# Kernel optimization log

Hardware: AMD Instinct MI355X
Metric: run time of the kernel (lower is better)

The kernel has to match this reference:

```python
import jax, jax.numpy as jnp
import numpy as np
from jax import lax

V, T, B, E, H, L, K = 32000, 256, 32, 512, 256, 2, 17  # vocab, seq, batch, emb, hidden/dir, layers, tags


def _lstm_dir(x, mask, Wih, Whh, bih, bhh, reverse):
    """One-direction LSTM with packed-sequence semantics.
    x: [B,T,D], mask: [B,T] bool. Padded steps do not update (h,c); padded outputs are 0."""
    Bs, Ts, _ = x.shape
    Hs = Whh.shape[1]
    xg = jnp.einsum('btd,gd->btg', x, Wih) + bih  # precompute input contributions [B,T,4H]

    def step(carry, inp):
        h, c = carry
        xg_t, m_t = inp  # [B,4H], [B]
        g = xg_t + h @ Whh.T + bhh
        i, f, gg, o = jnp.split(g, 4, axis=-1)  # torch gate order: i, f, g, o
        i = jax.nn.sigmoid(i); f = jax.nn.sigmoid(f)
        gg = jnp.tanh(gg); o = jax.nn.sigmoid(o)
        c_new = f * c + i * gg
        h_new = o * jnp.tanh(c_new)
        m = m_t[:, None]
        h2 = jnp.where(m, h_new, h)
        c2 = jnp.where(m, c_new, c)
        out = jnp.where(m, h_new, jnp.zeros_like(h_new))
        return (h2, c2), out

    z = jnp.zeros((Bs, Hs), dtype=x.dtype)
    xs = (jnp.swapaxes(xg, 0, 1), mask.T)
    _, ys = lax.scan(step, (z, z), xs, reverse=reverse)
    return jnp.swapaxes(ys, 0, 1)  # [B,T,H]


def _bilstm(x, mask, Wih, Whh, bih, bhh):
    for l in range(Wih.shape[0]):
        f = _lstm_dir(x, mask, Wih[l, 0], Whh[l, 0], bih[l, 0], bhh[l, 0], reverse=False)
        b = _lstm_dir(x, mask, Wih[l, 1], Whh[l, 1], bih[l, 1], bhh[l, 1], reverse=True)
        x = jnp.concatenate([f, b], axis=-1)
    return x


def _crf_nll(logits, labels, mask, input_lens, trans, start, end):
    maskf = mask.astype(logits.dtype)
    # --- numerator: score of gold path (AllenNLP _joint_likelihood) ---
    emit = jnp.take_along_axis(logits, labels[..., None], axis=2)[..., 0]  # [B,T]
    emit_sum = (emit * maskf).sum(1)
    tr = trans[labels[:, :-1], labels[:, 1:]]  # [B,T-1]
    tr_sum = (tr * maskf[:, 1:]).sum(1)
    last_tags = jnp.take_along_axis(labels, (input_lens - 1)[:, None], axis=1)[:, 0]
    numerator = start[labels[:, 0]] + emit_sum + tr_sum + end[last_tags]
    # --- denominator: forward algorithm over time ---
    alpha0 = start[None, :] + logits[:, 0]  # [B,K]

    def step(alpha, inp):
        logit_t, m_t = inp  # [B,K], [B]
        inner = alpha[:, :, None] + trans[None] + logit_t[:, None, :]  # [B,K,K]
        new = jax.nn.logsumexp(inner, axis=1)
        alpha = jnp.where(m_t[:, None], new, alpha)
        return alpha, None

    xs = (jnp.swapaxes(logits[:, 1:], 0, 1), mask[:, 1:].T)
    alpha, _ = lax.scan(step, alpha0, xs)
    partition = jax.nn.logsumexp(alpha + end[None, :], axis=1)
    return -(numerator - partition).sum()


def setup_inputs() -> dict:
    key = jax.random.key(0)
    ks = jax.random.split(key, 10)
    lens = jax.random.randint(ks[0], (B,), 1, T + 1)
    src = jax.random.randint(ks[1], (B, T), 1, V)
    src = jnp.where(jnp.arange(T)[None, :] < lens[:, None], src, 0)  # pad_idx=0
    labels = jax.random.randint(ks[2], (B, T), 0, K)
    emb = (jax.random.normal(ks[3], (V, E)) * 0.05).at[0].set(0.0)  # padding_idx=0 row zeroed
    Wih = jax.random.normal(ks[4], (L, 2, 4 * H, E)) * 0.05
    Whh = jax.random.normal(ks[5], (L, 2, 4 * H, H)) * 0.05
    bih = jnp.zeros((L, 2, 4 * H))
    bhh = jnp.zeros((L, 2, 4 * H))
    Wlin = jax.random.normal(ks[6], (K, 2 * H)) * 0.05
    blin = jnp.zeros((K,))
    trans = jax.random.normal(ks[7], (K, K)) * 0.05
    start = jax.random.normal(ks[8], (K,)) * 0.05
    end = jax.random.normal(ks[9], (K,)) * 0.05
    return dict(src=src, input_lens=lens, labels=labels, decode=0, emb=emb,
                Wih=Wih, Whh=Whh, bih=bih, bhh=bhh, Wlin=Wlin, blin=blin,
                trans=trans, start=start, end=end)


def reference(src, input_lens, labels, decode, emb, Wih, Whh, bih, bhh, Wlin, blin, trans, start, end):
    mask = src != 0  # create_mask with pad_idx=0
    x = emb[src]  # embedding lookup (dropout p=0 -> identity)
    feats = _bilstm(x, mask, Wih, Whh, bih, bhh)
    logits = feats @ Wlin.T + blin  # [B,T,K]
    # decode=False path: loss = -crf log-likelihood (summed over batch)
    return _crf_nll(logits, labels, mask, input_lens, trans, start, end)
```

## Files before the change

### kernel.cpp

```cpp
#include <hip/hip_runtime.h>

#define TT 256
#define BB 32
#define EE 512
#define HH 256
#define GG 1024
#define NK 17

typedef __attribute__((ext_vector_type(8))) short bf16x8;
typedef __attribute__((ext_vector_type(4))) float f32x4;

#if __has_builtin(__builtin_amdgcn_sdot8)
#define HAS_DOT8 1
#else
#define HAS_DOT8 0
#endif

__device__ __forceinline__ int dot4i8(int a, int b, int c) {
#if __has_builtin(__builtin_amdgcn_sdot4)
  return __builtin_amdgcn_sdot4(a, b, c, false);
#else
  int r = c;
#pragma unroll
  for (int e = 0; e < 4; ++e) {
    int av = (a << (24 - 8 * e)) >> 24;
    int bv = (b << (24 - 8 * e)) >> 24;
    r += av * bv;
  }
  return r;
#endif
}

__device__ __forceinline__ int dot8i4(int a, int b, int c) {
#if HAS_DOT8
  return __builtin_amdgcn_sdot8(a, b, c, false);
#else
  int alo = (a << 4) & (int)0xF0F0F0F0, ahi = a & (int)0xF0F0F0F0;
  int blo = (b << 4) & (int)0xF0F0F0F0, bhi = b & (int)0xF0F0F0F0;
  c = dot4i8(alo, blo, c);
  return dot4i8(ahi, bhi, c);
#endif
}

__device__ __forceinline__ short f2bf(float f) {
  unsigned int u = __float_as_uint(f);
  unsigned int rounding = 0x7FFFu + ((u >> 16) & 1u);
  return (short)((u + rounding) >> 16);
}
__device__ __forceinline__ float bfu2f_lo(unsigned int u) {
  return __uint_as_float(u << 16);
}
__device__ __forceinline__ float bfu2f_hi(unsigned int u) {
  return __uint_as_float(u & 0xFFFF0000u);
}
__device__ __forceinline__ float bfs2f(unsigned short us) {
  return __uint_as_float(((unsigned int)us) << 16);
}

__global__ void k_embed(const int* __restrict__ src,
                        const float* __restrict__ emb,
                        short* __restrict__ xb) {
  int row = blockIdx.x;
  int v = src[row];
  int t = threadIdx.x;
  const float4* e = reinterpret_cast<const float4*>(emb + (size_t)v * EE) + 2 * t;
  float4 a = e[0], b = e[1];
  bf16x8 r;
  r[0] = f2bf(a.x); r[1] = f2bf(a.y); r[2] = f2bf(a.z); r[3] = f2bf(a.w);
  r[4] = f2bf(b.x); r[5] = f2bf(b.y); r[6] = f2bf(b.z); r[7] = f2bf(b.w);
  *reinterpret_cast<bf16x8*>(xb + (size_t)row * EE + 8 * t) = r;
}

__global__ __launch_bounds__(256) void k_cvt(const float* __restrict__ in,
                                             short* __restrict__ out) {
  int i = (blockIdx.x * 256 + threadIdx.x) * 8;
  float4 a = *reinterpret_cast<const float4*>(in + i);
  float4 b = *reinterpret_cast<const float4*>(in + i + 4);
  bf16x8 r;
  r[0] = f2bf(a.x); r[1] = f2bf(a.y); r[2] = f2bf(a.z); r[3] = f2bf(a.w);
  r[4] = f2bf(b.x); r[5] = f2bf(b.y); r[6] = f2bf(b.z); r[7] = f2bf(b.w);
  *reinterpret_cast<bf16x8*>(out + i) = r;
}

__global__ __launch_bounds__(256) void k_quant4(const float* __restrict__ whh,
                                                const float* __restrict__ bih,
                                                const float* __restrict__ bhh,
                                                int* __restrict__ wq4,
                                                float* __restrict__ scl,
                                                float* __restrict__ biasb) {
  int wid = (blockIdx.x * 256 + threadIdx.x) >> 6;
  int lane = threadIdx.x & 63;
  int ld = wid >> 10, g = wid & 1023;
  float4 v = *reinterpret_cast<const float4*>(whh + (size_t)wid * HH + lane * 4);
  float m = fmaxf(fmaxf(fabsf(v.x), fabsf(v.y)), fmaxf(fabsf(v.z), fabsf(v.w)));
#pragma unroll
  for (int off = 32; off > 0; off >>= 1) m = fmaxf(m, __shfl_xor(m, off));
  m = fmaxf(m, 1e-20f);
  float inv = 7.f / m;
  unsigned q0 = (unsigned)((int)rintf(v.x * inv) & 0xF);
  unsigned q1 = (unsigned)((int)rintf(v.y * inv) & 0xF);
  unsigned q2 = (unsigned)((int)rintf(v.z * inv) & 0xF);
  unsigned q3 = (unsigned)((int)rintf(v.w * inv) & 0xF);
  unsigned bits = q0 | (q1 << 4) | (q2 << 8) | (q3 << 12);
  unsigned hi = __shfl_down(bits, 1);
  if (!(lane & 1)) {
    int kk = lane >> 1;
    wq4[(((size_t)ld * 8 + (kk >> 2)) * 1024 + g) * 4 + (kk & 3)] =
        (int)(bits | (hi << 16));
  }
  if (lane == 0) scl[wid] = m / 49.f;
  if (lane == 1) biasb[wid] = bih[wid] + bhh[wid];
}

__global__ __launch_bounds__(256) void k_gemm_mfma(
    const short* __restrict__ Xb,
    const short* __restrict__ Wb,
    const float* __restrict__ bias,
    unsigned short* __restrict__ out) {
  __shared__ short As[128][72];
  __shared__ short Bs[128][72];
  const int tid = threadIdx.x;
  const int wave = tid >> 6, lane = tid & 63;
  const int wr = wave >> 1, wc = wave & 1;
  const int m0 = blockIdx.y * 128, n0 = blockIdx.x * 128;
  f32x4 acc[4][4] = {};
  for (int k0 = 0; k0 < EE; k0 += 64) {
#pragma unroll
    for (int u = 0; u < 4; ++u) {
      int cid = u * 256 + tid;
      int row = cid >> 3, kc = cid & 7;
      *reinterpret_cast<int4*>(&As[row][kc * 8]) =
          *reinterpret_cast<const int4*>(Xb + (size_t)(m0 + row) * EE + k0 + kc * 8);
      *reinterpret_cast<int4*>(&Bs[row][kc * 8]) =
          *reinterpret_cast<const int4*>(Wb + (size_t)(n0 + row) * EE + k0 + kc * 8);
    }
    __syncthreads();
#pragma unroll
    for (int ko = 0; ko < 2; ++ko) {
      bf16x8 af[4], bff[4];
#pragma unroll
      for (int mi = 0; mi < 4; ++mi)
        af[mi] = *reinterpret_cast<const bf16x8*>(
            &As[wr * 64 + mi * 16 + (lane & 15)][ko * 32 + (lane >> 4) * 8]);
#pragma unroll
      for (int ni = 0; ni < 4; ++ni)
        bff[ni] = *reinterpret_cast<const bf16x8*>(
            &Bs[wc * 64 + ni * 16 + (lane & 15)][ko * 32 + (lane >> 4) * 8]);
#pragma unroll
      for (int mi = 0; mi < 4; ++mi)
#pragma unroll
        for (int ni = 0; ni < 4; ++ni)
          acc[mi][ni] = __builtin_amdgcn_mfma_f32_16x16x32_bf16(af[mi], bff[ni], acc[mi][ni], 0, 0, 0);
    }
    __syncthreads();
  }
  const int r0 = (lane >> 4) * 4, cc = lane & 15;
#pragma unroll
  for (int mi = 0; mi < 4; ++mi)
#pragma unroll
    for (int ni = 0; ni < 4; ++ni) {
      int gcol = n0 + wc * 64 + ni * 16 + cc;
      int dir = gcol >> 10, gg = gcol & 1023;
      float bv = bias[gcol];
      unsigned short* ob = out + (size_t)dir * (BB * TT * GG) + gg;
#pragma unroll
      for (int j = 0; j < 4; ++j) {
        int m = m0 + wr * 64 + mi * 16 + r0 + j;
        ob[(size_t)m * GG] = (unsigned short)f2bf(acc[mi][ni][j] + bv);
      }
    }
}

__global__ __launch_bounds__(1024) void k_rec(
    const unsigned short* __restrict__ xg,
    const uint4* __restrict__ wq4,
    const float* __restrict__ scl,
    const int* __restrict__ lens,
    short* __restrict__ outx)
{
  __shared__ __align__(16) int hq[32];
  const int bid = blockIdx.x;
  const int b = bid & 31;
  const int dir = bid >> 5;
  const int g = threadIdx.x;
  const uint4* wp = wq4 + (size_t)dir * (8 * 1024) + g;
  if (g < 32) hq[g] = 0;
#if HAS_DOT8
  const float f = scl[dir * 1024 + g];
#else
  const float f = scl[dir * 1024 + g] * (1.f / 256.f);
#endif
  __shared__ float pre[GG];
  const int len = lens[b];
  const unsigned short* xgb = xg + ((size_t)dir * (BB * TT) + (size_t)b * TT) * GG + g;
  float c = 0.f;
  __syncthreads();
  for (int s = 0; s < TT; ++s) {
    const int t = dir ? (TT - 1 - s) : s;
    float xv = bfs2f(xgb[(size_t)t * GG]);
    const uint4* h4 = reinterpret_cast<const uint4*>(hq);
    uint4 hv0 = h4[0], hv1 = h4[1], hv2 = h4[2], hv3 = h4[3];
    uint4 hv4 = h4[4], hv5 = h4[5], hv6 = h4[6], hv7 = h4[7];
    int acc = 0;
#define DOTQ(Q, HV)                                \
    { uint4 wv = wp[(Q) * 1024];                   \
      acc = dot8i4((int)wv.x, (int)HV.x, acc);     \
      acc = dot8i4((int)wv.y, (int)HV.y, acc);     \
      acc = dot8i4((int)wv.z, (int)HV.z, acc);     \
      acc = dot8i4((int)wv.w, (int)HV.w, acc); }
    DOTQ(0, hv0) DOTQ(1, hv1) DOTQ(2, hv2) DOTQ(3, hv3)
    DOTQ(4, hv4) DOTQ(5, hv5) DOTQ(6, hv6) DOTQ(7, hv7)
#undef DOTQ
    pre[g] = xv + (float)acc * f;
    __syncthreads();
    if (g < HH) {
      float gi = pre[g], gf = pre[HH + g], g2 = pre[2 * HH + g], go = pre[3 * HH + g];
      float iv = 1.f / (1.f + __expf(-gi));
      float fv = 1.f / (1.f + __expf(-gf));
      float e2 = __expf(fminf(2.f * g2, 80.f));
      float gv = (e2 - 1.f) / (e2 + 1.f);
      float ov = 1.f / (1.f + __expf(-go));
      float cn = fv * c + iv * gv;
      float e2c = __expf(fminf(2.f * cn, 80.f));
      float th = (e2c - 1.f) / (e2c + 1.f);
      float hn = ov * th;
      const bool m = (t < len);
      outx[((size_t)(b * TT) + t) * (2 * HH) + dir * HH + g] = f2bf(m ? hn : 0.f);
      if (m) {
        c = cn;
        int nib = ((int)rintf(hn * 7.f)) & 0xF;
        int pn = __shfl_xor(nib, 1);
        if (!(g & 1))
          reinterpret_cast<char*>(hq)[g >> 1] = (char)(nib | (pn << 4));
      }
    }
    __syncthreads();
  }
}

__global__ __launch_bounds__(256) void k_logits(
    const short* __restrict__ feats,
    const float* __restrict__ wlin,
    const float* __restrict__ blin,
    float* __restrict__ logits) {
  int o = blockIdx.x * 256 + threadIdx.x;
  int m = o / NK, jj = o - m * NK;
  const uint4* fr = reinterpret_cast<const uint4*>(feats + (size_t)m * EE);
  const float4* wr = reinterpret_cast<const float4*>(wlin + (size_t)jj * EE);
  float s = blin[jj];
  for (int q = 0; q < EE / 8; ++q) {
    uint4 fv = fr[q];
    float4 w0 = wr[2 * q], w1 = wr[2 * q + 1];
    s = fmaf(bfu2f_lo(fv.x), w0.x, s);
    s = fmaf(bfu2f_hi(fv.x), w0.y, s);
    s = fmaf(bfu2f_lo(fv.y), w0.z, s);
    s = fmaf(bfu2f_hi(fv.y), w0.w, s);
    s = fmaf(bfu2f_lo(fv.z), w1.x, s);
    s = fmaf(bfu2f_hi(fv.z), w1.y, s);
    s = fmaf(bfu2f_lo(fv.w), w1.z, s);
    s = fmaf(bfu2f_hi(fv.w), w1.w, s);
  }
  logits[o] = s;
}

__global__ __launch_bounds__(64) void k_crf(
    const float* __restrict__ logits,
    const int* __restrict__ labels,
    const int* __restrict__ lens,
    const float* __restrict__ trans,
    const float* __restrict__ startv,
    const float* __restrict__ endv,
    float* __restrict__ res) {
  const int b = blockIdx.x;
  const int tid = threadIdx.x;
  __shared__ float trs[NK * NK];
  __shared__ float alpha[NK];
  for (int i = tid; i < NK * NK; i += 64) trs[i] = trans[i];
  const int len = lens[b];
  const int* lab = labels + b * TT;
  const float* lg = logits + (size_t)b * TT * NK;
  float part = 0.f;
  for (int t = tid; t < TT; t += 64)
    if (t < len) part += lg[t * NK + lab[t]];
  for (int t = tid; t < TT - 1; t += 64)
    if (t + 1 < len) part += trs[lab[t] * NK + lab[t + 1]];
#pragma unroll
  for (int off = 32; off > 0; off >>= 1) part += __shfl_down(part, off);
  if (tid < NK) alpha[tid] = startv[tid] + lg[tid];
  const int tmax = (len < TT) ? len : TT;
  for (int t = 1; t < tmax; ++t) {
    float nv = 0.f;
    if (tid < NK) {
      float mxv = -1e30f;
#pragma unroll
      for (int i = 0; i < NK; ++i) mxv = fmaxf(mxv, alpha[i] + trs[i * NK + tid]);
      float sum = 0.f;
#pragma unroll
      for (int i = 0; i < NK; ++i) sum += __expf(alpha[i] + trs[i * NK + tid] - mxv);
      nv = mxv + __logf(sum) + lg[t * NK + tid];
    }
    if (tid < NK) alpha[tid] = nv;
  }
  if (tid == 0) {
    float mxv = -1e30f;
    float av[NK];
    for (int i = 0; i < NK; ++i) { av[i] = alpha[i] + endv[i]; mxv = fmaxf(mxv, av[i]); }
    float sum = 0.f;
    for (int i = 0; i < NK; ++i) sum += __expf(av[i] - mxv);
    float partition = mxv + __logf(sum);
    float numer = startv[lab[0]] + part + endv[lab[len - 1]];
    res[b] = numer - partition;
  }
}

__global__ void k_final(const float* __restrict__ res, float* __restrict__ out) {
  int tid = threadIdx.x;
  float v = (tid < BB) ? res[tid] : 0.f;
#pragma unroll
  for (int off = 32; off > 0; off >>= 1) v += __shfl_down(v, off);
  if (tid == 0) out[0] = -v;
}

extern "C" void kernel_launch(void* const* d_in, const int* in_sizes, int n_in,
                              void* d_out, int out_size, void* d_ws, size_t ws_size,
                              hipStream_t stream) {
  const int* src = (const int*)d_in[0];
  const int* lens = (const int*)d_in[1];
  const int* labels = (const int*)d_in[2];
  const float* emb = (const float*)d_in[4];
  const float* Wih = (const float*)d_in[5];
  const float* Whh = (const float*)d_in[6];
  const float* bih = (const float*)d_in[7];
  const float* bhh = (const float*)d_in[8];
  const float* Wlin = (const float*)d_in[9];
  const float* blin = (const float*)d_in[10];
  const float* trans = (const float*)d_in[11];
  const float* startv = (const float*)d_in[12];
  const float* endv = (const float*)d_in[13];

  char* w = (char*)d_ws;
  short* xb0 = (short*)w;   w += (size_t)BB * TT * EE * 2;
  short* xb1 = (short*)w;   w += (size_t)BB * TT * EE * 2;
  short* xb2 = (short*)w;   w += (size_t)BB * TT * EE * 2;
  unsigned short* xg = (unsigned short*)w; w += (size_t)2 * BB * TT * GG * 2;
  int* wq4 = (int*)w;       w += (size_t)4 * 32 * 1024 * 4;
  float* scl = (float*)w;   w += (size_t)4 * 1024 * 4;
  float* biasb = (float*)w; w += (size_t)2 * 2 * GG * 4;
  float* logits = (float*)w; w += (size_t)BB * TT * NK * 4;
  float* res = (float*)w;   w += 256;
  short* wbb = (short*)w;   w += (size_t)4 * GG * EE * 2;

  k_embed<<<BB * TT, 64, 0, stream>>>(src, emb, xb0);
  k_quant4<<<1024, 256, 0, stream>>>(Whh, bih, bhh, wq4, scl, biasb);
  k_cvt<<<(4 * GG * EE) / (256 * 8), 256, 0, stream>>>(Wih, wbb);

  const short* xin[2] = {xb0, xb1};
  short* xout[2] = {xb1, xb2};
  for (int l = 0; l < 2; ++l) {
    k_gemm_mfma<<<dim3(2 * GG / 128, (BB * TT) / 128), 256, 0, stream>>>(
        xin[l], wbb + (size_t)l * 2 * GG * EE, biasb + l * 2 * GG, xg);
    k_rec<<<64, 1024, 0, stream>>>(
        xg, reinterpret_cast<const uint4*>(wq4) + (size_t)l * 2 * 8 * 1024,
        scl + (size_t)l * 2 * 1024, lens, xout[l]);
  }

  k_logits<<<(BB * TT * NK) / 256, 256, 0, stream>>>(xb2, Wlin, blin, logits);
  k_crf<<<BB, 64, 0, stream>>>(logits, labels, lens, trans, startv, endv, res);
  k_final<<<1, 64, 0, stream>>>(res, (float*)d_out);
}
```

Measured before the change: 597.1 us.

## Keep int4 recurrent weights in registers and compute all four gates per hidden unit

```diff
diff --git a/kernel.cpp b/kernel.cpp
--- a/kernel.cpp
+++ b/kernel.cpp
@@ -91,6 +91,7 @@
   int wid = (blockIdx.x * 256 + threadIdx.x) >> 6;
   int lane = threadIdx.x & 63;
   int ld = wid >> 10, g = wid & 1023;
+  int gate = g >> 8, j = g & 255;
   float4 v = *reinterpret_cast<const float4*>(whh + (size_t)wid * HH + lane * 4);
   float m = fmaxf(fmaxf(fabsf(v.x), fabsf(v.y)), fmaxf(fabsf(v.z), fabsf(v.w)));
 #pragma unroll
@@ -105,7 +106,10 @@
   unsigned hi = __shfl_down(bits, 1);
   if (!(lane & 1)) {
     int kk = lane >> 1;
-    wq4[(((size_t)ld * 8 + (kk >> 2)) * 1024 + g) * 4 + (kk & 3)] =
+    int kq = kk >> 3, ld8 = kk & 7;
+    int tid_dest = j * 4 + kq;
+    int cch = gate * 2 + (ld8 >> 2), dw = ld8 & 3;
+    wq4[(size_t)ld * 32768 + ((size_t)(cch * 1024 + tid_dest) << 2) + dw] =
         (int)(bits | (hi << 16));
   }
   if (lane == 0) scl[wid] = m / 49.f;
@@ -178,62 +182,103 @@
     const int* __restrict__ lens,
     short* __restrict__ outx)
 {
-  __shared__ __align__(16) int hq[32];
+  __shared__ __align__(16) int hq2[2][32];
   const int bid = blockIdx.x;
   const int b = bid & 31;
   const int dir = bid >> 5;
-  const int g = threadIdx.x;
-  const uint4* wp = wq4 + (size_t)dir * (8 * 1024) + g;
-  if (g < 32) hq[g] = 0;
+  const int tid = threadIdx.x;
+  const int j = tid >> 2;
+  const uint4* wp = wq4 + (size_t)dir * 8192 + tid;
+  uint4 w0 = wp[0];
+  uint4 w1 = wp[1024];
+  uint4 w2 = wp[2048];
+  uint4 w3 = wp[3072];
+  uint4 w4 = wp[4096];
+  uint4 w5 = wp[5120];
+  uint4 w6 = wp[6144];
+  uint4 w7 = wp[7168];
+  if (tid < 64) ((int*)hq2)[tid] = 0;
 #if HAS_DOT8
-  const float f = scl[dir * 1024 + g];
+  const float fsc = 1.f;
 #else
-  const float f = scl[dir * 1024 + g] * (1.f / 256.f);
+  const float fsc = 1.f / 256.f;
 #endif
-  __shared__ float pre[GG];
+  const float s0 = scl[dir * 1024 + j] * fsc;
+  const float s1 = scl[dir * 1024 + 256 + j] * fsc;
+  const float s2 = scl[dir * 1024 + 512 + j] * fsc;
+  const float s3 = scl[dir * 1024 + 768 + j] * fsc;
   const int len = lens[b];
-  const unsigned short* xgb = xg + ((size_t)dir * (BB * TT) + (size_t)b * TT) * GG + g;
-  float c = 0.f;
+  const unsigned short* xgb = xg + ((size_t)dir * (BB * TT) + (size_t)b * TT) * GG;
+  float c = 0.f, hcur = 0.f;
   __syncthreads();
   for (int s = 0; s < TT; ++s) {
     const int t = dir ? (TT - 1 - s) : s;
-    float xv = bfs2f(xgb[(size_t)t * GG]);
-    const uint4* h4 = reinterpret_cast<const uint4*>(hq);
-    uint4 hv0 = h4[0], hv1 = h4[1], hv2 = h4[2], hv3 = h4[3];
-    uint4 hv4 = h4[4], hv5 = h4[5], hv6 = h4[6], hv7 = h4[7];
-    int acc = 0;
-#define DOTQ(Q, HV)                                \
-    { uint4 wv = wp[(Q) * 1024];                   \
-      acc = dot8i4((int)wv.x, (int)HV.x, acc);     \
-      acc = dot8i4((int)wv.y, (int)HV.y, acc);     \
-      acc = dot8i4((int)wv.z, (int)HV.z, acc);     \
-      acc = dot8i4((int)wv.w, (int)HV.w, acc); }
-    DOTQ(0, hv0) DOTQ(1, hv1) DOTQ(2, hv2) DOTQ(3, hv3)
-    DOTQ(4, hv4) DOTQ(5, hv5) DOTQ(6, hv6) DOTQ(7, hv7)
-#undef DOTQ
-    pre[g] = xv + (float)acc * f;
-    __syncthreads();
-    if (g < HH) {
-      float gi = pre[g], gf = pre[HH + g], g2 = pre[2 * HH + g], go = pre[3 * HH + g];
-      float iv = 1.f / (1.f + __expf(-gi));
-      float fv = 1.f / (1.f + __expf(-gf));
-      float e2 = __expf(fminf(2.f * g2, 80.f));
-      float gv = (e2 - 1.f) / (e2 + 1.f);
-      float ov = 1.f / (1.f + __expf(-go));
-      float cn = fv * c + iv * gv;
-      float e2c = __expf(fminf(2.f * cn, 80.f));
-      float th = (e2c - 1.f) / (e2c + 1.f);
-      float hn = ov * th;
-      const bool m = (t < len);
-      outx[((size_t)(b * TT) + t) * (2 * HH) + dir * HH + g] = f2bf(m ? hn : 0.f);
-      if (m) {
-        c = cn;
-        int nib = ((int)rintf(hn * 7.f)) & 0xF;
-        int pn = __shfl_xor(nib, 1);
-        if (!(g & 1))
-          reinterpret_cast<char*>(hq)[g >> 1] = (char)(nib | (pn << 4));
-      }
-    }
+    const unsigned short* xrow = xgb + (size_t)t * GG;
+    float xv0 = bfs2f(xrow[j]);
+    float xv1 = bfs2f(xrow[256 + j]);
+    float xv2 = bfs2f(xrow[512 + j]);
+    float xv3 = bfs2f(xrow[768 + j]);
+    const int p = s & 1;
+    const uint4* hv4 = reinterpret_cast<const uint4*>(hq2[p]);
+    uint4 h0 = hv4[(tid & 3) * 2], h1 = hv4[(tid & 3) * 2 + 1];
+    int a0 = 0, a1 = 0, a2 = 0, a3 = 0;
+    a0 = dot8i4((int)w0.x, (int)h0.x, a0);
+    a0 = dot8i4((int)w0.y, (int)h0.y, a0);
+    a0 = dot8i4((int)w0.z, (int)h0.z, a0);
+    a0 = dot8i4((int)w0.w, (int)h0.w, a0);
+    a0 = dot8i4((int)w1.x, (int)h1.x, a0);
+    a0 = dot8i4((int)w1.y, (int)h1.y, a0);
+    a0 = dot8i4((int)w1.z, (int)h1.z, a0);
+    a0 = dot8i4((int)w1.w, (int)h1.w, a0);
+    a1 = dot8i4((int)w2.x, (int)h0.x, a1);
+    a1 = dot8i4((int)w2.y, (int)h0.y, a1);
+    a1 = dot8i4((int)w2.z, (int)h0.z, a1);
+    a1 = dot8i4((int)w2.w, (int)h0.w, a1);
+    a1 = dot8i4((int)w3.x, (int)h1.x, a1);
+    a1 = dot8i4((int)w3.y, (int)h1.y, a1);
+    a1 = dot8i4((int)w3.z, (int)h1.z, a1);
+    a1 = dot8i4((int)w3.w, (int)h1.w, a1);
+    a2 = dot8i4((int)w4.x, (int)h0.x, a2);
+    a2 = dot8i4((int)w4.y, (int)h0.y, a2);
+    a2 = dot8i4((int)w4.z, (int)h0.z, a2);
+    a2 = dot8i4((int)w4.w, (int)h0.w, a2);
+    a2 = dot8i4((int)w5.x, (int)h1.x, a2);
+    a2 = dot8i4((int)w5.y, (int)h1.y, a2);
+    a2 = dot8i4((int)w5.z, (int)h1.z, a2);
+    a2 = dot8i4((int)w5.w, (int)h1.w, a2);
+    a3 = dot8i4((int)w6.x, (int)h0.x, a3);
+    a3 = dot8i4((int)w6.y, (int)h0.y, a3);
+    a3 = dot8i4((int)w6.z, (int)h0.z, a3);
+    a3 = dot8i4((int)w6.w, (int)h0.w, a3);
+    a3 = dot8i4((int)w7.x, (int)h1.x, a3);
+    a3 = dot8i4((int)w7.y, (int)h1.y, a3);
+    a3 = dot8i4((int)w7.z, (int)h1.z, a3);
+    a3 = dot8i4((int)w7.w, (int)h1.w, a3);
+    a0 += __shfl_xor(a0, 1); a0 += __shfl_xor(a0, 2);
+    a1 += __shfl_xor(a1, 1); a1 += __shfl_xor(a1, 2);
+    a2 += __shfl_xor(a2, 1); a2 += __shfl_xor(a2, 2);
+    a3 += __shfl_xor(a3, 1); a3 += __shfl_xor(a3, 2);
+    float gi = xv0 + (float)a0 * s0;
+    float gf = xv1 + (float)a1 * s1;
+    float gg = xv2 + (float)a2 * s2;
+    float go = xv3 + (float)a3 * s3;
+    float iv = 1.f / (1.f + __expf(-gi));
+    float fv = 1.f / (1.f + __expf(-gf));
+    float e2 = __expf(fminf(2.f * gg, 80.f));
+    float gv = (e2 - 1.f) / (e2 + 1.f);
+    float ov = 1.f / (1.f + __expf(-go));
+    float cn = fv * c + iv * gv;
+    float e2c = __expf(fminf(2.f * cn, 80.f));
+    float th = (e2c - 1.f) / (e2c + 1.f);
+    float hn = ov * th;
+    const bool m = (t < len);
+    if (m) { c = cn; hcur = hn; }
+    if ((tid & 3) == 0)
+      outx[((size_t)(b * TT) + t) * (2 * HH) + dir * HH + j] = f2bf(m ? hn : 0.f);
+    int nib = ((int)rintf(hcur * 7.f)) & 0xF;
+    int pn = __shfl_xor(nib, 4);
+    if ((tid & 7) == 0)
+      reinterpret_cast<char*>(hq2[p ^ 1])[tid >> 3] = (char)(nib | (pn << 4));
     __syncthreads();
   }
 }
@@ -343,7 +388,7 @@
   short* xb1 = (short*)w;   w += (size_t)BB * TT * EE * 2;
   short* xb2 = (short*)w;   w += (size_t)BB * TT * EE * 2;
   unsigned short* xg = (unsigned short*)w; w += (size_t)2 * BB * TT * GG * 2;
-  int* wq4 = (int*)w;       w += (size_t)4 * 32 * 1024 * 4;
+  int* wq4 = (int*)w;       w += (size_t)4 * 32768 * 4;
   float* scl = (float*)w;   w += (size_t)4 * 1024 * 4;
   float* biasb = (float*)w; w += (size_t)2 * 2 * GG * 4;
   float* logits = (float*)w; w += (size_t)BB * TT * NK * 4;
@@ -360,7 +405,7 @@
     k_gemm_mfma<<<dim3(2 * GG / 128, (BB * TT) / 128), 256, 0, stream>>>(
         xin[l], wbb + (size_t)l * 2 * GG * EE, biasb + l * 2 * GG, xg);
     k_rec<<<64, 1024, 0, stream>>>(
-        xg, reinterpret_cast<const uint4*>(wq4) + (size_t)l * 2 * 8 * 1024,
+        xg, reinterpret_cast<const uint4*>(wq4) + (size_t)l * 2 * 8192,
         scl + (size_t)l * 2 * 1024, lens, xout[l]);
   }
 
```

New measurement: 860.2 us. +44.1%, slower.

## Halve recurrent block size with two gate rows per thread; merge embed and weight-convert kernels

Applied to the files above, without the earlier changes.

```diff
diff --git a/kernel.cpp b/kernel.cpp
--- a/kernel.cpp
+++ b/kernel.cpp
@@ -57,29 +57,30 @@
   return __uint_as_float(((unsigned int)us) << 16);
 }
 
-__global__ void k_embed(const int* __restrict__ src,
-                        const float* __restrict__ emb,
-                        short* __restrict__ xb) {
-  int row = blockIdx.x;
-  int v = src[row];
+__global__ void k_prep_x(const int* __restrict__ src,
+                         const float* __restrict__ emb,
+                         const float* __restrict__ Wih,
+                         short* __restrict__ xb,
+                         short* __restrict__ wbb) {
+  int blk = blockIdx.x;
   int t = threadIdx.x;
-  const float4* e = reinterpret_cast<const float4*>(emb + (size_t)v * EE) + 2 * t;
-  float4 a = e[0], b = e[1];
-  bf16x8 r;
-  r[0] = f2bf(a.x); r[1] = f2bf(a.y); r[2] = f2bf(a.z); r[3] = f2bf(a.w);
-  r[4] = f2bf(b.x); r[5] = f2bf(b.y); r[6] = f2bf(b.z); r[7] = f2bf(b.w);
-  *reinterpret_cast<bf16x8*>(xb + (size_t)row * EE + 8 * t) = r;
-}
-
-__global__ __launch_bounds__(256) void k_cvt(const float* __restrict__ in,
-                                             short* __restrict__ out) {
-  int i = (blockIdx.x * 256 + threadIdx.x) * 8;
-  float4 a = *reinterpret_cast<const float4*>(in + i);
-  float4 b = *reinterpret_cast<const float4*>(in + i + 4);
-  bf16x8 r;
-  r[0] = f2bf(a.x); r[1] = f2bf(a.y); r[2] = f2bf(a.z); r[3] = f2bf(a.w);
-  r[4] = f2bf(b.x); r[5] = f2bf(b.y); r[6] = f2bf(b.z); r[7] = f2bf(b.w);
-  *reinterpret_cast<bf16x8*>(out + i) = r;
+  if (blk < BB * TT) {
+    int v = src[blk];
+    const float4* e = reinterpret_cast<const float4*>(emb + (size_t)v * EE) + 2 * t;
+    float4 a = e[0], b = e[1];
+    bf16x8 r;
+    r[0] = f2bf(a.x); r[1] = f2bf(a.y); r[2] = f2bf(a.z); r[3] = f2bf(a.w);
+    r[4] = f2bf(b.x); r[5] = f2bf(b.y); r[6] = f2bf(b.z); r[7] = f2bf(b.w);
+    *reinterpret_cast<bf16x8*>(xb + (size_t)blk * EE + 8 * t) = r;
+  } else {
+    int i = ((blk - BB * TT) * 64 + t) * 8;
+    float4 a = *reinterpret_cast<const float4*>(Wih + i);
+    float4 b = *reinterpret_cast<const float4*>(Wih + i + 4);
+    bf16x8 r;
+    r[0] = f2bf(a.x); r[1] = f2bf(a.y); r[2] = f2bf(a.z); r[3] = f2bf(a.w);
+    r[4] = f2bf(b.x); r[5] = f2bf(b.y); r[6] = f2bf(b.z); r[7] = f2bf(b.w);
+    *reinterpret_cast<bf16x8*>(wbb + i) = r;
+  }
 }
 
 __global__ __launch_bounds__(256) void k_quant4(const float* __restrict__ whh,
@@ -171,50 +172,62 @@
     }
 }
 
-__global__ __launch_bounds__(1024) void k_rec(
+__global__ __launch_bounds__(512, 2) void k_rec(
     const unsigned short* __restrict__ xg,
     const uint4* __restrict__ wq4,
     const float* __restrict__ scl,
     const int* __restrict__ lens,
     short* __restrict__ outx)
 {
+  __shared__ float pre[GG];
   __shared__ __align__(16) int hq[32];
   const int bid = blockIdx.x;
   const int b = bid & 31;
   const int dir = bid >> 5;
-  const int g = threadIdx.x;
-  const uint4* wp = wq4 + (size_t)dir * (8 * 1024) + g;
-  if (g < 32) hq[g] = 0;
+  const int L = threadIdx.x;
+  const int g0 = L, g1 = L + 512;
+  const uint4* wp0 = wq4 + (size_t)dir * (8 * 1024) + g0;
+  const uint4* wp1 = wq4 + (size_t)dir * (8 * 1024) + g1;
+  if (L < 32) hq[L] = 0;
 #if HAS_DOT8
-  const float f = scl[dir * 1024 + g];
+  const float f0 = scl[dir * 1024 + g0];
+  const float f1 = scl[dir * 1024 + g1];
 #else
-  const float f = scl[dir * 1024 + g] * (1.f / 256.f);
+  const float f0 = scl[dir * 1024 + g0] * (1.f / 256.f);
+  const float f1 = scl[dir * 1024 + g1] * (1.f / 256.f);
 #endif
-  __shared__ float pre[GG];
   const int len = lens[b];
-  const unsigned short* xgb = xg + ((size_t)dir * (BB * TT) + (size_t)b * TT) * GG + g;
+  const unsigned short* xgb = xg + ((size_t)dir * (BB * TT) + (size_t)b * TT) * GG;
   float c = 0.f;
   __syncthreads();
   for (int s = 0; s < TT; ++s) {
     const int t = dir ? (TT - 1 - s) : s;
-    float xv = bfs2f(xgb[(size_t)t * GG]);
+    float xv0 = bfs2f(xgb[(size_t)t * GG + g0]);
+    float xv1 = bfs2f(xgb[(size_t)t * GG + g1]);
     const uint4* h4 = reinterpret_cast<const uint4*>(hq);
     uint4 hv0 = h4[0], hv1 = h4[1], hv2 = h4[2], hv3 = h4[3];
     uint4 hv4 = h4[4], hv5 = h4[5], hv6 = h4[6], hv7 = h4[7];
-    int acc = 0;
-#define DOTQ(Q, HV)                                \
-    { uint4 wv = wp[(Q) * 1024];                   \
-      acc = dot8i4((int)wv.x, (int)HV.x, acc);     \
-      acc = dot8i4((int)wv.y, (int)HV.y, acc);     \
-      acc = dot8i4((int)wv.z, (int)HV.z, acc);     \
-      acc = dot8i4((int)wv.w, (int)HV.w, acc); }
-    DOTQ(0, hv0) DOTQ(1, hv1) DOTQ(2, hv2) DOTQ(3, hv3)
-    DOTQ(4, hv4) DOTQ(5, hv5) DOTQ(6, hv6) DOTQ(7, hv7)
+    int a0 = 0, a1 = 0;
+#define DOTQ(WP, ACC, Q, HV)                               \
+    { uint4 wv = WP[(Q) * 1024];                           \
+      ACC = dot8i4((int)wv.x, (int)HV.x, ACC);             \
+      ACC = dot8i4((int)wv.y, (int)HV.y, ACC);             \
+      ACC = dot8i4((int)wv.z, (int)HV.z, ACC);             \
+      ACC = dot8i4((int)wv.w, (int)HV.w, ACC); }
+    DOTQ(wp0, a0, 0, hv0) DOTQ(wp0, a0, 1, hv1)
+    DOTQ(wp0, a0, 2, hv2) DOTQ(wp0, a0, 3, hv3)
+    DOTQ(wp0, a0, 4, hv4) DOTQ(wp0, a0, 5, hv5)
+    DOTQ(wp0, a0, 6, hv6) DOTQ(wp0, a0, 7, hv7)
+    DOTQ(wp1, a1, 0, hv0) DOTQ(wp1, a1, 1, hv1)
+    DOTQ(wp1, a1, 2, hv2) DOTQ(wp1, a1, 3, hv3)
+    DOTQ(wp1, a1, 4, hv4) DOTQ(wp1, a1, 5, hv5)
+    DOTQ(wp1, a1, 6, hv6) DOTQ(wp1, a1, 7, hv7)
 #undef DOTQ
-    pre[g] = xv + (float)acc * f;
+    pre[g0] = xv0 + (float)a0 * f0;
+    pre[g1] = xv1 + (float)a1 * f1;
     __syncthreads();
-    if (g < HH) {
-      float gi = pre[g], gf = pre[HH + g], g2 = pre[2 * HH + g], go = pre[3 * HH + g];
+    if (L < HH) {
+      float gi = pre[L], gf = pre[HH + L], g2 = pre[2 * HH + L], go = pre[3 * HH + L];
       float iv = 1.f / (1.f + __expf(-gi));
       float fv = 1.f / (1.f + __expf(-gf));
       float e2 = __expf(fminf(2.f * g2, 80.f));
@@ -225,13 +238,13 @@
       float th = (e2c - 1.f) / (e2c + 1.f);
       float hn = ov * th;
       const bool m = (t < len);
-      outx[((size_t)(b * TT) + t) * (2 * HH) + dir * HH + g] = f2bf(m ? hn : 0.f);
+      outx[((size_t)(b * TT) + t) * (2 * HH) + dir * HH + L] = f2bf(m ? hn : 0.f);
       if (m) {
         c = cn;
         int nib = ((int)rintf(hn * 7.f)) & 0xF;
         int pn = __shfl_xor(nib, 1);
-        if (!(g & 1))
-          reinterpret_cast<char*>(hq)[g >> 1] = (char)(nib | (pn << 4));
+        if (!(L & 1))
+          reinterpret_cast<char*>(hq)[L >> 1] = (char)(nib | (pn << 4));
       }
     }
     __syncthreads();
@@ -350,16 +363,16 @@
   float* res = (float*)w;   w += 256;
   short* wbb = (short*)w;   w += (size_t)4 * GG * EE * 2;
 
-  k_embed<<<BB * TT, 64, 0, stream>>>(src, emb, xb0);
+  k_prep_x<<<BB * TT + (4 * GG * EE) / (64 * 8), 64, 0, stream>>>(
+      src, emb, Wih, xb0, wbb);
   k_quant4<<<1024, 256, 0, stream>>>(Whh, bih, bhh, wq4, scl, biasb);
-  k_cvt<<<(4 * GG * EE) / (256 * 8), 256, 0, stream>>>(Wih, wbb);
 
   const short* xin[2] = {xb0, xb1};
   short* xout[2] = {xb1, xb2};
   for (int l = 0; l < 2; ++l) {
     k_gemm_mfma<<<dim3(2 * GG / 128, (BB * TT) / 128), 256, 0, stream>>>(
         xin[l], wbb + (size_t)l * 2 * GG * EE, biasb + l * 2 * GG, xg);
-    k_rec<<<64, 1024, 0, stream>>>(
+    k_rec<<<64, 512, 0, stream>>>(
         xg, reinterpret_cast<const uint4*>(wq4) + (size_t)l * 2 * 8 * 1024,
         scl + (size_t)l * 2 * 1024, lens, xout[l]);
   }
```

After: 589.9 us. Within noise of the previous version (-1.2%).
